# Performance work log

Hardware: AMD Instinct MI355X
Metric: run time of the kernel (lower is better)

The kernel has to match this reference:

```python
import jax, jax.numpy as jnp
import numpy as np
import math

EXP_HALF = math.exp(-0.5)  # constant scale exp(-1/2) from the original module


def setup_inputs() -> dict:
    key = jax.random.key(0)
    k1, k2, k3, k4 = jax.random.split(key, 4)
    T, N, DR2 = 32, 4096, 512
    all_data_static = jax.random.normal(k1, (T, N, DR2), dtype=jnp.float32)
    threshold_nc = jax.random.uniform(k2, (T, N, 1), dtype=jnp.float32)
    all_data_dynamic_now = jax.random.uniform(k3, (N, DR2), dtype=jnp.float32)
    # w1 initialized RandomNormal(mean=1.0, stddev=0.5) as in build()
    w1 = 1.0 + 0.5 * jax.random.normal(k4, (2 * DR2, DR2), dtype=jnp.float32)
    smooth_gate_logit = jnp.full((1,), -0.5, dtype=jnp.float32)
    smooth_scale = jnp.full((1,), 0.5, dtype=jnp.float32)
    return {
        "all_data_static": all_data_static,
        "threshold_nc": threshold_nc,
        "all_data_dynamic_now": all_data_dynamic_now,
        "w1": w1,
        "smooth_gate_logit": smooth_gate_logit,
        "smooth_scale": smooth_scale,
    }


def _evolve(all_data_static, threshold_nc, h0, w1, smooth_gate_logit, smooth_scale):
    def step(h, inputs):
        s_i, thr_i = inputs  # s_i: [N, DR2], thr_i: [N, 1]
        z = jnp.concatenate([h, s_i], axis=-1) @ w1  # [N, DR2]
        cand = jax.nn.sigmoid(z * thr_i + h * (1.0 - thr_i)) * EXP_HALF
        delta = jnp.mean(jnp.abs(cand - h), axis=-1, keepdims=True)  # [N, 1]
        g = jax.nn.sigmoid(smooth_gate_logit + smooth_scale * delta)
        h_new = g * h + (1.0 - g) * cand
        return h_new, h_new

    _, states = jax.lax.scan(step, h0, (all_data_static, threshold_nc))
    # states: [T, N, DR2] -- state after each of the T gated updates
    all_data_dynamic = states
    h_final = states[-1]
    all_data_dynamic_diff = states[1:] - states[:-1]  # [T-1, N, DR2]
    return all_data_dynamic, h_final, all_data_dynamic_diff


def reference(all_data_static, threshold_nc, all_data_dynamic_now, w1,
              smooth_gate_logit, smooth_scale):
    return _evolve(all_data_static, threshold_nc, all_data_dynamic_now, w1,
                   smooth_gate_logit, smooth_scale)
```

## Files before the change

kernel.cpp:

```cpp
#include <hip/hip_runtime.h>

typedef __attribute__((ext_vector_type(4))) float f32x4;

#define T_STEPS 32
#define T_LDS   16
#define NROWS 4096
#define DR2 512
#define EXP_HALF 0.6065306597126334f

#define OUT_HFINAL 67108864ul
#define OUT_DIFF   69206016ul
#define SLOT_F32   2097152ul

__device__ __forceinline__ unsigned char f2fp8(float f) {
  return (unsigned char)__builtin_amdgcn_cvt_pk_fp8_f32(f, f, 0, false);
}

__device__ __forceinline__ void barrier_lds() {
  asm volatile("s_waitcnt lgkmcnt(0)" ::: "memory");
  __builtin_amdgcn_s_barrier();
  asm volatile("" ::: "memory");
}

__device__ __forceinline__ float* zs_slot(float* out, int t) {
  return out + (t < 31 ? OUT_DIFF + (size_t)t * SLOT_F32 : OUT_HFINAL);
}
__device__ __forceinline__ unsigned char* zs_blk8(float* out, int t, int eb) {
  return (unsigned char*)zs_slot(out, t) + (size_t)eb * 32768;
}


__global__ __launch_bounds__(256) void quant_w1(const float* __restrict__ w1,
                                                unsigned char* __restrict__ w1f) {
  const int half = blockIdx.x >> 5;
  const int ct   = blockIdx.x & 31;
  const int l15  = threadIdx.x & 15;
  const int kk   = threadIdx.x >> 4;
  const int col  = ct * 16 + l15;
  const int K0   = half * 512;
#pragma unroll
  for (int lg = 0; lg < 4; lg++) {
    unsigned long long v = 0;
#pragma unroll
    for (int e = 0; e < 8; e++) {
      int k = K0 + kk * 32 + lg * 8 + e;
      unsigned long long b = f2fp8(w1[(size_t)k * 512 + col]);
      v |= b << (8 * e);
    }
    *(unsigned long long*)(w1f + (size_t)half * 262144 + ct * 8192 + kk * 512
                           + lg * 128 + l15 * 8) = v;
  }
}

__global__ __attribute__((amdgpu_flat_work_group_size(1024, 1024),
                          amdgpu_waves_per_eu(4, 4)))
void evolve_fused(
    const float* __restrict__ s_all,
    const float* __restrict__ thr_all,
    const float* __restrict__ h0,
    const unsigned char* __restrict__ w1f,
    const float* __restrict__ p_logit,
    const float* __restrict__ p_scale,
    float* __restrict__ out)
{
  __shared__ __align__(16) unsigned char zs_lds[T_LDS * 8192];
  __shared__ __align__(16) unsigned char A_lds[2][8192];
  __shared__ float thr_lds[T_STEPS * 16];
  __shared__ float partial[16][17];

  const int tid  = threadIdx.x;
  const int lane = tid & 63;
  const int wave = tid >> 6;
  const int l15  = lane & 15;
  const int lg   = lane >> 4;
  const int brow0 = blockIdx.x * 16;
  const int colbase = wave * 32 + l15;

  if (tid < T_STEPS * 16)
    thr_lds[tid] = thr_all[(size_t)(tid >> 4) * NROWS + brow0 + (tid & 15)];

  long Bv[2][16];
#pragma unroll
  for (int n = 0; n < 2; n++)
#pragma unroll
    for (int kk = 0; kk < 16; kk++)
      Bv[n][kk] = *(const long*)(w1f + 262144
                   + (size_t)(wave * 2 + n) * 8192 + kk * 512 + lane * 8);

  const int di = (lane >> 2) * 512 + (lane & 3) * 128
               + ((wave ^ l15) & 15) * 8;
  const float* sbase = s_all + ((size_t)brow0 + wave) * DR2 + lane * 8;

  float4 v0 = *(const float4*)sbase;
  float4 v1 = *(const float4*)(sbase + 4);
  {
    int pa = __builtin_amdgcn_cvt_pk_fp8_f32(v0.x, v0.y, 0, false);
    int pw0 = __builtin_amdgcn_cvt_pk_fp8_f32(v0.z, v0.w, pa, true);
    int pb = __builtin_amdgcn_cvt_pk_fp8_f32(v1.x, v1.y, 0, false);
    int pw1 = __builtin_amdgcn_cvt_pk_fp8_f32(v1.z, v1.w, pb, true);
    *(uint2*)(A_lds[0] + di) = make_uint2((unsigned)pw0, (unsigned)pw1);
  }
  barrier_lds();

#pragma unroll 2
  for (int t = 0; t < T_STEPS; t++) {
    if (t < T_STEPS - 1) {
      const float* p = sbase + (size_t)(t + 1) * NROWS * DR2;
      v0 = *(const float4*)p;
      v1 = *(const float4*)(p + 4);
    }
    f32x4 acc[2];
#pragma unroll
    for (int n = 0; n < 2; n++)
#pragma unroll
      for (int i = 0; i < 4; i++) acc[n][i] = -256.0f;
    const unsigned char* buf = A_lds[t & 1];
#pragma unroll
    for (int kk = 0; kk < 16; kk++) {
      long a = *(const long*)(buf + kk * 512 + lg * 128
                              + ((l15 ^ ((kk * 4 + lg) & 15)) << 3));
      acc[0] = __builtin_amdgcn_mfma_f32_16x16x32_fp8_fp8(a, Bv[0][kk], acc[0], 0, 0, 0);
      acc[1] = __builtin_amdgcn_mfma_f32_16x16x32_fp8_fp8(a, Bv[1][kk], acc[1], 0, 0, 0);
    }
    int p0 = __builtin_amdgcn_cvt_pk_fp8_f32(acc[0][0], acc[0][1], 0, false);
    p0 = __builtin_amdgcn_cvt_pk_fp8_f32(acc[0][2], acc[0][3], p0, true);
    int p1 = __builtin_amdgcn_cvt_pk_fp8_f32(acc[1][0], acc[1][1], 0, false);
    p1 = __builtin_amdgcn_cvt_pk_fp8_f32(acc[1][2], acc[1][3], p1, true);

    if (t < T_STEPS - 1) {
      int pa = __builtin_amdgcn_cvt_pk_fp8_f32(v0.x, v0.y, 0, false);
      int pw0 = __builtin_amdgcn_cvt_pk_fp8_f32(v0.z, v0.w, pa, true);
      int pb = __builtin_amdgcn_cvt_pk_fp8_f32(v1.x, v1.y, 0, false);
      int pw1 = __builtin_amdgcn_cvt_pk_fp8_f32(v1.z, v1.w, pb, true);
      *(uint2*)(A_lds[(t + 1) & 1] + di) = make_uint2((unsigned)pw0, (unsigned)pw1);
    }
    if (t < T_LDS)
      *(uint2*)(zs_lds + t * 8192 + (size_t)tid * 8) =
          make_uint2((unsigned)p0, (unsigned)p1);
    else
      *(uint2*)(zs_blk8(out, t, blockIdx.x) + (size_t)tid * 8) =
          make_uint2((unsigned)p0, (unsigned)p1);
    barrier_lds();
  }

#pragma unroll
  for (int n = 0; n < 2; n++)
#pragma unroll
    for (int kk = 0; kk < 16; kk++)
      Bv[n][kk] = *(const long*)(w1f + (size_t)(wave * 2 + n) * 8192
                                 + kk * 512 + lane * 8);

  f32x4 h[2];
#pragma unroll
  for (int n = 0; n < 2; n++)
#pragma unroll
    for (int i = 0; i < 4; i++)
      h[n][i] = h0[(size_t)(brow0 + lg * 4 + i) * DR2 + colbase + n * 16];

  const float glogit = *p_logit;
  const float gscale = *p_scale;

  uint2 zraw = make_uint2(0u, 0u), znext = make_uint2(0u, 0u);

#pragma unroll 1
  for (int t = 0; t < T_STEPS; t++) {
#pragma unroll
    for (int n = 0; n < 2; n++) {
      int c = colbase + n * 16;
      int base = (c >> 5) * 512 + ((c >> 3) & 3) * 128 + (c & 7);
      int x = (c >> 3) & 15;
#pragma unroll
      for (int i = 0; i < 4; i++) {
        int r = lg * 4 + i;
        A_lds[0][base + ((r ^ x) & 15) * 8] = f2fp8(h[n][i]);
      }
    }
    if (t + 1 >= T_LDS && t + 1 < T_STEPS)
      znext = *(const uint2*)(zs_blk8(out, t + 1, blockIdx.x) + (size_t)tid * 8);
    barrier_lds();

    f32x4 acc[2];
#pragma unroll
    for (int n = 0; n < 2; n++)
#pragma unroll
      for (int i = 0; i < 4; i++) acc[n][i] = 256.0f;
#pragma unroll
    for (int kk = 0; kk < 16; kk++) {
      long a = *(const long*)(A_lds[0] + kk * 512 + lg * 128
                              + ((l15 ^ ((kk * 4 + lg) & 15)) << 3));
      acc[0] = __builtin_amdgcn_mfma_f32_16x16x32_fp8_fp8(a, Bv[0][kk], acc[0], 0, 0, 0);
      acc[1] = __builtin_amdgcn_mfma_f32_16x16x32_fp8_fp8(a, Bv[1][kk], acc[1], 0, 0, 0);
    }
    uint2 zr;
    if (t < T_LDS)
      zr = *(const uint2*)(zs_lds + t * 8192 + (size_t)tid * 8);
    else
      zr = zraw;
    {
      const unsigned int zw[2] = { zr.x, zr.y };
#pragma unroll
      for (int j = 0; j < 8; j++) {
        unsigned int b = (zw[j >> 2] >> ((j & 3) * 8)) & 0xffu;
        unsigned int man = (b & 0x7fu) << 20;
        unsigned int bits = ((b & 0x80u) << 24) | (man + (120u << 23));
        acc[j >> 2][j & 3] += __uint_as_float(bits);
      }
    }

    f32x4 cand[2];
#pragma unroll
    for (int i = 0; i < 4; i++) {
      int r = lg * 4 + i;
      float th = thr_lds[t * 16 + r];
      float s = 0.f;
#pragma unroll
      for (int n = 0; n < 2; n++) {
        float hh = h[n][i];
        float x  = acc[n][i] * th + hh * (1.0f - th);
        float c  = EXP_HALF / (1.0f + __expf(-x));
        cand[n][i] = c;
        s += fabsf(c - hh);
      }
      s += __shfl_xor(s, 1);
      s += __shfl_xor(s, 2);
      s += __shfl_xor(s, 4);
      s += __shfl_xor(s, 8);
      if (l15 == 0) partial[r][wave] = s;
    }
    barrier_lds();

    float tot = partial[l15][lg] + partial[l15][lg + 4]
              + partial[l15][lg + 8] + partial[l15][lg + 12];
    tot += __shfl_xor(tot, 16);
    tot += __shfl_xor(tot, 32);
    float gme = 1.0f / (1.0f + __expf(-(glogit + gscale * (tot * (1.0f / 512.0f)))));

    const size_t srowbase = (size_t)t * NROWS + brow0;
#pragma unroll
    for (int i = 0; i < 4; i++) {
      int r = lg * 4 + i;
      float g = __shfl(gme, r);
#pragma unroll
      for (int n = 0; n < 2; n++) {
        int c = colbase + n * 16;
        float hh = h[n][i];
        float hn = g * hh + (1.0f - g) * cand[n][i];
        h[n][i] = hn;
        out[(srowbase + r) * DR2 + c] = hn;
        if (t > 0) out[OUT_DIFF + (srowbase - NROWS + r) * DR2 + c] = hn - hh;
      }
    }
    if (t == T_STEPS - 1) {
#pragma unroll
      for (int i = 0; i < 4; i++) {
        int r = lg * 4 + i;
#pragma unroll
        for (int n = 0; n < 2; n++)
          out[OUT_HFINAL + (size_t)(brow0 + r) * DR2 + colbase + n * 16] = h[n][i];
      }
    }
    zraw = znext;
  }
}

extern "C" void kernel_launch(void* const* d_in, const int* in_sizes, int n_in,
                              void* d_out, int out_size, void* d_ws, size_t ws_size,
                              hipStream_t stream) {
  const float* s_all   = (const float*)d_in[0];
  const float* thr_all = (const float*)d_in[1];
  const float* h0      = (const float*)d_in[2];
  const float* w1      = (const float*)d_in[3];
  const float* p_logit = (const float*)d_in[4];
  const float* p_scale = (const float*)d_in[5];
  float* out = (float*)d_out;

  unsigned char* w1f = (unsigned char*)d_ws;

  hipLaunchKernelGGL(quant_w1, dim3(64), dim3(256), 0, stream, w1, w1f);
  hipLaunchKernelGGL(evolve_fused, dim3(256), dim3(1024), 0, stream,
                     s_all, thr_all, h0, w1f, p_logit, p_scale, out);
}
```

Measured before the change: 258.1 us.

## Prefetch static inputs two steps ahead and fuse h staging into update

The first (static GEMM) phase now runs two timesteps per iteration. Both LDS A buffers are staged together, and the global loads for the next pair of timesteps are issued two steps ahead, so load latency is hidden better. In the recurrent phase, the fp8 write of the new h into LDS moves into the gating update loop, and the barrier moves to the end of each step. This removes a separate store pass at the top of the loop. The cost is more live registers for the prefetched float4s and more LDS write dependencies around the barriers.

```diff
diff --git a/kernel.cpp b/kernel.cpp
--- a/kernel.cpp
+++ b/kernel.cpp
@@ -51,6 +51,14 @@
                            + lg * 128 + l15 * 8) = v;
   }
 }
+
+#define STAGE(bufp, u0, u1) do {                                              \
+    int _pa  = __builtin_amdgcn_cvt_pk_fp8_f32((u0).x, (u0).y, 0, false);     \
+    int _pw0 = __builtin_amdgcn_cvt_pk_fp8_f32((u0).z, (u0).w, _pa, true);    \
+    int _pb  = __builtin_amdgcn_cvt_pk_fp8_f32((u1).x, (u1).y, 0, false);     \
+    int _pw1 = __builtin_amdgcn_cvt_pk_fp8_f32((u1).z, (u1).w, _pb, true);    \
+    *(uint2*)((bufp) + di) = make_uint2((unsigned)_pw0, (unsigned)_pw1);      \
+  } while (0)
 
 __global__ __attribute__((amdgpu_flat_work_group_size(1024, 1024),
                           amdgpu_waves_per_eu(4, 4)))
@@ -91,57 +99,68 @@
                + ((wave ^ l15) & 15) * 8;
   const float* sbase = s_all + ((size_t)brow0 + wave) * DR2 + lane * 8;
 
-  float4 v0 = *(const float4*)sbase;
-  float4 v1 = *(const float4*)(sbase + 4);
+  float4 a0 = *(const float4*)sbase;
+  float4 a1 = *(const float4*)(sbase + 4);
   {
-    int pa = __builtin_amdgcn_cvt_pk_fp8_f32(v0.x, v0.y, 0, false);
-    int pw0 = __builtin_amdgcn_cvt_pk_fp8_f32(v0.z, v0.w, pa, true);
-    int pb = __builtin_amdgcn_cvt_pk_fp8_f32(v1.x, v1.y, 0, false);
-    int pw1 = __builtin_amdgcn_cvt_pk_fp8_f32(v1.z, v1.w, pb, true);
-    *(uint2*)(A_lds[0] + di) = make_uint2((unsigned)pw0, (unsigned)pw1);
+    const float* p1 = sbase + (size_t)NROWS * DR2;
+    float4 b0 = *(const float4*)p1;
+    float4 b1 = *(const float4*)(p1 + 4);
+    STAGE(A_lds[0], a0, a1);
+    STAGE(A_lds[1], b0, b1);
+  }
+  float4 c0, c1, d0, d1;
+  {
+    const float* p2 = sbase + (size_t)2 * NROWS * DR2;
+    c0 = *(const float4*)p2;  c1 = *(const float4*)(p2 + 4);
+    const float* p3 = sbase + (size_t)3 * NROWS * DR2;
+    d0 = *(const float4*)p3;  d1 = *(const float4*)(p3 + 4);
   }
   barrier_lds();
 
-#pragma unroll 2
-  for (int t = 0; t < T_STEPS; t++) {
-    if (t < T_STEPS - 1) {
-      const float* p = sbase + (size_t)(t + 1) * NROWS * DR2;
-      v0 = *(const float4*)p;
-      v1 = *(const float4*)(p + 4);
-    }
-    f32x4 acc[2];
-#pragma unroll
-    for (int n = 0; n < 2; n++)
-#pragma unroll
-      for (int i = 0; i < 4; i++) acc[n][i] = -256.0f;
-    const unsigned char* buf = A_lds[t & 1];
-#pragma unroll
-    for (int kk = 0; kk < 16; kk++) {
-      long a = *(const long*)(buf + kk * 512 + lg * 128
-                              + ((l15 ^ ((kk * 4 + lg) & 15)) << 3));
-      acc[0] = __builtin_amdgcn_mfma_f32_16x16x32_fp8_fp8(a, Bv[0][kk], acc[0], 0, 0, 0);
-      acc[1] = __builtin_amdgcn_mfma_f32_16x16x32_fp8_fp8(a, Bv[1][kk], acc[1], 0, 0, 0);
-    }
-    int p0 = __builtin_amdgcn_cvt_pk_fp8_f32(acc[0][0], acc[0][1], 0, false);
-    p0 = __builtin_amdgcn_cvt_pk_fp8_f32(acc[0][2], acc[0][3], p0, true);
-    int p1 = __builtin_amdgcn_cvt_pk_fp8_f32(acc[1][0], acc[1][1], 0, false);
-    p1 = __builtin_amdgcn_cvt_pk_fp8_f32(acc[1][2], acc[1][3], p1, true);
-
-    if (t < T_STEPS - 1) {
-      int pa = __builtin_amdgcn_cvt_pk_fp8_f32(v0.x, v0.y, 0, false);
-      int pw0 = __builtin_amdgcn_cvt_pk_fp8_f32(v0.z, v0.w, pa, true);
-      int pb = __builtin_amdgcn_cvt_pk_fp8_f32(v1.x, v1.y, 0, false);
-      int pw1 = __builtin_amdgcn_cvt_pk_fp8_f32(v1.z, v1.w, pb, true);
-      *(uint2*)(A_lds[(t + 1) & 1] + di) = make_uint2((unsigned)pw0, (unsigned)pw1);
-    }
-    if (t < T_LDS)
-      *(uint2*)(zs_lds + t * 8192 + (size_t)tid * 8) =
-          make_uint2((unsigned)p0, (unsigned)p1);
-    else
-      *(uint2*)(zs_blk8(out, t, blockIdx.x) + (size_t)tid * 8) =
-          make_uint2((unsigned)p0, (unsigned)p1);
-    barrier_lds();
-  }
+#pragma unroll 1
+  for (int p = 0; p < T_STEPS / 2; p++) {
+    const int t0 = 2 * p;
+#pragma unroll
+    for (int q = 0; q < 2; q++) {
+      const int t = t0 + q;
+      const unsigned char* buf = A_lds[q];
+      f32x4 acc[2];
+#pragma unroll
+      for (int n = 0; n < 2; n++)
+#pragma unroll
+        for (int i = 0; i < 4; i++) acc[n][i] = -256.0f;
+#pragma unroll
+      for (int kk = 0; kk < 16; kk++) {
+        long a = *(const long*)(buf + kk * 512 + lg * 128
+                                + ((l15 ^ ((kk * 4 + lg) & 15)) << 3));
+        acc[0] = __builtin_amdgcn_mfma_f32_16x16x32_fp8_fp8(a, Bv[0][kk], acc[0], 0, 0, 0);
+        acc[1] = __builtin_amdgcn_mfma_f32_16x16x32_fp8_fp8(a, Bv[1][kk], acc[1], 0, 0, 0);
+      }
+      int z0 = __builtin_amdgcn_cvt_pk_fp8_f32(acc[0][0], acc[0][1], 0, false);
+      z0 = __builtin_amdgcn_cvt_pk_fp8_f32(acc[0][2], acc[0][3], z0, true);
+      int z1 = __builtin_amdgcn_cvt_pk_fp8_f32(acc[1][0], acc[1][1], 0, false);
+      z1 = __builtin_amdgcn_cvt_pk_fp8_f32(acc[1][2], acc[1][3], z1, true);
+      if (t < T_LDS)
+        *(uint2*)(zs_lds + t * 8192 + (size_t)tid * 8) =
+            make_uint2((unsigned)z0, (unsigned)z1);
+      else
+        *(uint2*)(zs_blk8(out, t, blockIdx.x) + (size_t)tid * 8) =
+            make_uint2((unsigned)z0, (unsigned)z1);
+    }
+    if (p < T_STEPS / 2 - 1) {
+      barrier_lds();
+      STAGE(A_lds[0], c0, c1);
+      STAGE(A_lds[1], d0, d1);
+      if (p < T_STEPS / 2 - 2) {
+        const float* pc = sbase + (size_t)(t0 + 4) * NROWS * DR2;
+        c0 = *(const float4*)pc;  c1 = *(const float4*)(pc + 4);
+        const float* pd = sbase + (size_t)(t0 + 5) * NROWS * DR2;
+        d0 = *(const float4*)pd;  d1 = *(const float4*)(pd + 4);
+      }
+      barrier_lds();
+    }
+  }
+  barrier_lds();
 
 #pragma unroll
   for (int n = 0; n < 2; n++)
@@ -157,27 +176,25 @@
     for (int i = 0; i < 4; i++)
       h[n][i] = h0[(size_t)(brow0 + lg * 4 + i) * DR2 + colbase + n * 16];
 
+#pragma unroll
+  for (int n = 0; n < 2; n++) {
+    int c = colbase + n * 16;
+    int base = (c >> 5) * 512 + ((c >> 3) & 3) * 128 + (c & 7);
+    int x = (c >> 3) & 15;
+#pragma unroll
+    for (int i = 0; i < 4; i++)
+      A_lds[0][base + (((lg * 4 + i) ^ x) & 15) * 8] = f2fp8(h[n][i]);
+  }
+
   const float glogit = *p_logit;
   const float gscale = *p_scale;
-
   uint2 zraw = make_uint2(0u, 0u), znext = make_uint2(0u, 0u);
+  barrier_lds();
 
 #pragma unroll 1
   for (int t = 0; t < T_STEPS; t++) {
-#pragma unroll
-    for (int n = 0; n < 2; n++) {
-      int c = colbase + n * 16;
-      int base = (c >> 5) * 512 + ((c >> 3) & 3) * 128 + (c & 7);
-      int x = (c >> 3) & 15;
-#pragma unroll
-      for (int i = 0; i < 4; i++) {
-        int r = lg * 4 + i;
-        A_lds[0][base + ((r ^ x) & 15) * 8] = f2fp8(h[n][i]);
-      }
-    }
     if (t + 1 >= T_LDS && t + 1 < T_STEPS)
       znext = *(const uint2*)(zs_blk8(out, t + 1, blockIdx.x) + (size_t)tid * 8);
-    barrier_lds();
 
     f32x4 acc[2];
 #pragma unroll
@@ -246,6 +263,9 @@
         float hh = h[n][i];
         float hn = g * hh + (1.0f - g) * cand[n][i];
         h[n][i] = hn;
+        int base = (c >> 5) * 512 + ((c >> 3) & 3) * 128 + (c & 7);
+        int x = (c >> 3) & 15;
+        A_lds[0][base + ((r ^ x) & 15) * 8] = f2fp8(hn);
         out[(srowbase + r) * DR2 + c] = hn;
         if (t > 0) out[OUT_DIFF + (srowbase - NROWS + r) * DR2 + c] = hn - hh;
       }
@@ -259,6 +279,7 @@
           out[OUT_HFINAL + (size_t)(brow0 + r) * DR2 + colbase + n * 16] = h[n][i];
       }
     }
+    barrier_lds();
     zraw = znext;
   }
 }
```

Measured after the change: 366.8 us. +42.1%, slower.
